# Kernel optimization log

Measured on AMD Instinct MI355X. Metric: run time of the kernel, lower is better.

The kernel has to match this reference:

```python
import jax, jax.numpy as jnp
import numpy as np

B, H, S, D = 4, 16, 1024, 64


def setup_inputs() -> dict:
    key = jax.random.key(0)
    kq, kk, kv, kw = jax.random.split(key, 4)
    xq = jax.random.normal(kq, (B, H, S, D), dtype=jnp.float32)
    xk = jax.random.normal(kk, (B, H, S, D), dtype=jnp.float32)
    xv = jax.random.normal(kv, (B, H, S, D), dtype=jnp.float32)
    # wpsm: nn.Linear(n_heads, n_heads, bias=False) weight, shape [H_out, H_in]
    bound = 1.0 / np.sqrt(H)
    W = jax.random.uniform(kw, (H, H), minval=-bound, maxval=bound, dtype=jnp.float32)
    return {"xq": xq, "xk": xk, "xv": xv, "W": W, "causal": 1}


def reference(xq, xk, xv, W, causal):
    head_dim = xq.shape[-1]
    sq, sk = xq.shape[-2], xk.shape[-2]
    # QK^T scaled: [B, H, Sq, Sk]
    scores = jnp.einsum("bhqd,bhkd->bhqk", xq, xk) * jax.lax.rsqrt(jnp.float32(head_dim))
    # head-mixing linear over head axis: mixed[b,g,q,k] = sum_h W[g,h] * scores[b,h,q,k]
    scores = jnp.einsum("gh,bhqk->bgqk", W, scores)
    if causal:
        mask = jnp.triu(jnp.full((sq, sk), -jnp.inf, dtype=scores.dtype), k=1)
        scores = scores + mask  # broadcast over [B, H]
    probs = jax.nn.softmax(scores.astype(jnp.float32), axis=-1).astype(xq.dtype)
    out = jnp.einsum("bhqk,bhkd->bhqd", probs, xv)
    return out.transpose(0, 2, 1, 3)  # [B, Sq, H, D]
```

## Files before the change

### kernel.cpp

```cpp
#include <hip/hip_runtime.h>
#include <math.h>

#define NB 4
#define HH 16
#define SS 1024
#define DD 64
#define NKST 16

typedef __attribute__((ext_vector_type(8))) short bf16x8;
typedef __attribute__((ext_vector_type(4))) float f32x4;

static __device__ __forceinline__ short f2bf(float f) {
    __bf16 h = (__bf16)f;
    return __builtin_bit_cast(short, h);
}
static __device__ __forceinline__ float bflo(int w) {
    return __builtin_bit_cast(float, (unsigned)w << 16);
}
static __device__ __forceinline__ float bfhi(int w) {
    return __builtin_bit_cast(float, (unsigned)w & 0xffff0000u);
}
static __device__ __forceinline__ int pidx(int pos, int hp) {
    int s = ((pos >> 2) & 3) | (((pos >> 9) & 1) << 2);
    return pos * 8 + (hp ^ s);
}
static __device__ __forceinline__ int midx(int gl, int loc, int x3) {
    return gl * 512 + ((((loc >> 2) ^ x3) << 2) | (loc & 3));
}

static __device__ __forceinline__ bf16x8 load8_bf16(const float* p) {
    const float4* p4 = reinterpret_cast<const float4*>(p);
    float4 a = p4[0], b = p4[1];
    bf16x8 f;
    f[0]=f2bf(a.x); f[1]=f2bf(a.y); f[2]=f2bf(a.z); f[3]=f2bf(a.w);
    f[4]=f2bf(b.x); f[5]=f2bf(b.y); f[6]=f2bf(b.z); f[7]=f2bf(b.w);
    return f;
}

__global__ __launch_bounds__(256) void prep_kfrag(const float* __restrict__ xk,
                                                  short* __restrict__ kfr) {
    int c = blockIdx.x * 256 + threadIdx.x;
    int lane = c & 63, ds = (c >> 6) & 1, kt = (c >> 7) & 3;
    int kst = (c >> 9) & 15, h = (c >> 13) & 15, b = c >> 17;
    const float* src = xk + ((size_t)((b * HH + h) * SS) + kst * 64 + kt * 16 + (lane & 15)) * DD
                          + ds * 32 + (lane >> 4) * 8;
    *(reinterpret_cast<bf16x8*>(kfr) + c) = load8_bf16(src);
}

__global__ __launch_bounds__(256) void prep_vfrag(const float* __restrict__ xv,
                                                  short* __restrict__ vfr) {
    __shared__ float T[64][65];
    int tile = blockIdx.x;
    int t = threadIdx.x;
    const float* src = xv + ((size_t)(tile >> 4) * SS + (tile & 15) * 64) * DD;
    int row = t >> 2, col = (t & 3) * 16;
#pragma unroll
    for (int ii = 0; ii < 4; ++ii) {
        float4 v = *reinterpret_cast<const float4*>(src + row * DD + col + ii * 4);
        T[row][col + ii*4] = v.x; T[row][col + ii*4 + 1] = v.y;
        T[row][col + ii*4 + 2] = v.z; T[row][col + ii*4 + 3] = v.w;
    }
    __syncthreads();
#pragma unroll
    for (int jj = 0; jj < 2; ++jj) {
        int c2 = t * 2 + jj;
        int lane = c2 & 63, nt = (c2 >> 6) & 3, kc = (c2 >> 8) & 1;
        bf16x8 o;
#pragma unroll
        for (int i = 0; i < 8; ++i)
            o[i] = f2bf(T[kc * 32 + (lane >> 4) * 8 + i][nt * 16 + (lane & 15)]);
        *(reinterpret_cast<bf16x8*>(vfr) + (size_t)tile * 512 + c2) = o;
    }
}

__global__ __launch_bounds__(512, 4) void hca_fused(
    const float* __restrict__ xq, const short* __restrict__ kfr,
    const short* __restrict__ vfr, const float* __restrict__ Wm,
    const int* __restrict__ causalp, float* __restrict__ out)
{
    __shared__ int Pbuf[8192];
    __shared__ int Mbuf[4096];

    const int tid  = threadIdx.x;
    const int lane = tid & 63;
    const int w    = tid >> 6;
    const int l15  = lane & 15;
    const int lg   = lane >> 4;

    const int bid  = blockIdx.x;
    const int i8   = bid & 255;
    const int rnd  = bid >> 8;
    const int b    = i8 & 3;
    const int jj   = i8 >> 2;
    const int qt   = rnd ? jj : 63 - jj;
    const int half = rnd;
    const int q0   = qt << 4;

    const int causal = causalp[0];
    const int g  = half * 8 + w;

    const float LOG2E = 1.44269504088896f;

    bf16x8 wt = {0,0,0,0,0,0,0,0};
    if (lg < 2) {
#pragma unroll
        for (int i = 0; i < 8; ++i)
            wt[i] = f2bf(Wm[l15 * 16 + lg * 8 + i] * 0.125f * LOG2E);
    }

    bf16x8 qf[2][2];
#pragma unroll
    for (int hi = 0; hi < 2; ++hi) {
        const float* qp = xq + ((size_t)(b * HH + 2 * w + hi) * SS + q0 + l15) * DD + lg * 8;
#pragma unroll
        for (int ds = 0; ds < 2; ++ds) qf[hi][ds] = load8_bf16(qp + ds * 32);
    }

    f32x4 oacc[4];
#pragma unroll
    for (int nt = 0; nt < 4; ++nt) oacc[nt] = (f32x4){0.f, 0.f, 0.f, 0.f};
    float mrun = -INFINITY, lrun = 0.f;

    const int nk = causal ? ((q0 + 16 + 63) >> 6) : NKST;

    for (int kst = 0; kst < nk; ++kst) {
        const int k0 = kst << 6;

        const short* kbase = kfr + ((size_t)((b * HH + 2 * w) * NKST + kst) * 8) * 512 + lane * 8;
#pragma unroll
        for (int kt = 0; kt < 4; ++kt) {
            f32x4 a0 = (f32x4){0.f,0.f,0.f,0.f}, a1 = a0;
#pragma unroll
            for (int ds = 0; ds < 2; ++ds) {
                bf16x8 kfa = *reinterpret_cast<const bf16x8*>(kbase + (kt*2 + ds) * 512);
                bf16x8 kfb = *reinterpret_cast<const bf16x8*>(kbase + (NKST*8 + kt*2 + ds) * 512);
                a0 = __builtin_amdgcn_mfma_f32_16x16x32_bf16(qf[0][ds], kfa, a0, 0, 0, 0);
                a1 = __builtin_amdgcn_mfma_f32_16x16x32_bf16(qf[1][ds], kfb, a1, 0, 0, 0);
            }
#pragma unroll
            for (int r = 0; r < 4; ++r) {
                int pos = (lg * 4 + r) * 64 + kt * 16 + l15;
                int pk = (int)(unsigned short)f2bf(a0[r]) | ((int)(unsigned short)f2bf(a1[r]) << 16);
                Pbuf[pidx(pos, w)] = pk;
            }
        }

        const short* vbase = vfr + ((size_t)((b * HH + g) * NKST + kst) * 8) * 512 + lane * 8;
        bf16x8 vf[8];
#pragma unroll
        for (int kc = 0; kc < 2; ++kc)
#pragma unroll
            for (int nt = 0; nt < 4; ++nt)
                vf[kc * 4 + nt] = *reinterpret_cast<const bf16x8*>(vbase + (kc*4 + nt) * 512);

        __syncthreads();

#pragma unroll
        for (int m = 0; m < 8; ++m) {
            const int c = w * 8 + m;
            const int pos = c * 16 + l15;
            int4 ia = {0, 0, 0, 0};
            if (lg < 2) {
                ia.x = Pbuf[pidx(pos, lg * 4 + 0)];
                ia.y = Pbuf[pidx(pos, lg * 4 + 1)];
                ia.z = Pbuf[pidx(pos, lg * 4 + 2)];
                ia.w = Pbuf[pidx(pos, lg * 4 + 3)];
            }
            bf16x8 A = __builtin_bit_cast(bf16x8, ia);
            f32x4 cc = (f32x4){0.f, 0.f, 0.f, 0.f};
            cc = __builtin_amdgcn_mfma_f32_16x16x32_bf16(A, wt, cc, 0, 0, 0);
            if ((l15 >> 3) == half) {
                int q = c >> 2;
                int loc = q * 32 + (c & 3) * 8 + lg * 2;
                int x3 = (q + l15) & 7;
                int u0 = (int)(unsigned short)f2bf(cc[0]) | ((int)(unsigned short)f2bf(cc[1]) << 16);
                int u1 = (int)(unsigned short)f2bf(cc[2]) | ((int)(unsigned short)f2bf(cc[3]) << 16);
                *reinterpret_cast<int2*>(&Mbuf[midx(l15 & 7, loc, x3)]) = make_int2(u0, u1);
            }
        }
        __syncthreads();

        const int x3r = (l15 + w) & 7;
        int4 rA = *reinterpret_cast<const int4*>(&Mbuf[midx(w, l15 * 32 + lg * 4, x3r)]);
        int4 rB = *reinterpret_cast<const int4*>(&Mbuf[midx(w, l15 * 32 + 16 + lg * 4, x3r)]);

        float sm[16];
#pragma unroll
        for (int j = 0; j < 4; ++j) {
            sm[2*j]     = bflo(rA[j]);  sm[2*j + 1] = bfhi(rA[j]);
            sm[8 + 2*j] = bflo(rB[j]);  sm[9 + 2*j] = bfhi(rB[j]);
        }
        if (causal && kst == nk - 1) {
#pragma unroll
            for (int j = 0; j < 16; ++j) {
                int kk = (j < 8) ? (lg * 8 + j) : (32 + lg * 8 + (j - 8));
                if (k0 + kk > q0 + l15) sm[j] = -INFINITY;
            }
        }

        float mx[4];
#pragma unroll
        for (int t = 0; t < 4; ++t)
            mx[t] = fmaxf(fmaxf(sm[4*t], sm[4*t+1]), fmaxf(sm[4*t+2], sm[4*t+3]));
        float mt = fmaxf(fmaxf(mx[0], mx[1]), fmaxf(mx[2], mx[3]));
        mt = fmaxf(mt, __shfl_xor(mt, 16));
        mt = fmaxf(mt, __shfl_xor(mt, 32));

        if (__any(mt > mrun + 8.0f)) {
            float mnew = fmaxf(mrun, mt);
            float scl = __builtin_amdgcn_exp2f(mrun - mnew);
            mrun = mnew;
            lrun *= scl;
            int scli = __builtin_bit_cast(int, scl);
#pragma unroll
            for (int r = 0; r < 4; ++r) {
                int v = __builtin_amdgcn_ds_bpermute((lg * 4 + r) * 4, scli);
                float s = __builtin_bit_cast(float, v);
#pragma unroll
                for (int nt = 0; nt < 4; ++nt) oacc[nt][r] *= s;
            }
        }

        float p[16];
#pragma unroll
        for (int j = 0; j < 16; ++j) p[j] = __builtin_amdgcn_exp2f(sm[j] - mrun);
        float s0 = ((p[0]+p[1]) + (p[2]+p[3])) + ((p[4]+p[5]) + (p[6]+p[7]));
        float s1 = ((p[8]+p[9]) + (p[10]+p[11])) + ((p[12]+p[13]) + (p[14]+p[15]));
        lrun += s0 + s1;

        int paw[8];
#pragma unroll
        for (int t = 0; t < 8; ++t)
            paw[t] = (int)(unsigned short)f2bf(p[2*t]) | ((int)(unsigned short)f2bf(p[2*t+1]) << 16);
        bf16x8 pa0 = __builtin_bit_cast(bf16x8, *(int4*)&paw[0]);
        bf16x8 pa1 = __builtin_bit_cast(bf16x8, *(int4*)&paw[4]);

#pragma unroll
        for (int nt = 0; nt < 4; ++nt) {
            oacc[nt] = __builtin_amdgcn_mfma_f32_16x16x32_bf16(pa0, vf[nt], oacc[nt], 0, 0, 0);
            oacc[nt] = __builtin_amdgcn_mfma_f32_16x16x32_bf16(pa1, vf[4 + nt], oacc[nt], 0, 0, 0);
        }
    }

    float lt = lrun;
    lt += __shfl_xor(lt, 16);
    lt += __shfl_xor(lt, 32);
    int lti = __builtin_bit_cast(int, lt);
#pragma unroll
    for (int r = 0; r < 4; ++r) {
        int v = __builtin_amdgcn_ds_bpermute((lg * 4 + r) * 4, lti);
        float linv = 1.0f / __builtin_bit_cast(float, v);
        int q = lg * 4 + r;
#pragma unroll
        for (int nt = 0; nt < 4; ++nt)
            out[((size_t)(b * SS + q0 + q) * HH + g) * DD + nt * 16 + l15] =
                oacc[nt][r] * linv;
    }
}

extern "C" void kernel_launch(void* const* d_in, const int* in_sizes, int n_in,
                              void* d_out, int out_size, void* d_ws, size_t ws_size,
                              hipStream_t stream) {
    const float* xq = (const float*)d_in[0];
    const float* xk = (const float*)d_in[1];
    const float* xv = (const float*)d_in[2];
    const float* Wm = (const float*)d_in[3];
    const int* causal = (const int*)d_in[4];
    float* out = (float*)d_out;

    short* vfr = (short*)d_ws;
    short* kfr = vfr + (size_t)NB * HH * SS * DD;

    prep_kfrag<<<2048, 256, 0, stream>>>(xk, kfr);
    prep_vfrag<<<NB * HH * NKST, 256, 0, stream>>>(xv, vfr);

    hca_fused<<<512, 512, 0, stream>>>(xq, kfr, vfr, Wm, causal, out);
}
```

Baseline: 87.75 us.

## Split key range across blocks with split-K attention and a combine kernel

Before, each block handled half the output heads and recomputed the full QK and head-mix for its q-tile. Now each block computes all 16 heads but only every other key tile (even or odd). It writes bf16 partial outputs plus per-row max and sum to workspace, and a new combine kernel merges the two halves. This removes the duplicated QK and head-mix work across the two blocks. It also evens out the causal imbalance between blocks, and s_setprio hints are added around the MFMA sections. The cost is a doubled Mbuf in shared memory, an extra kernel launch, more workspace traffic, and extra bf16 rounding of the partial outputs.

```diff
diff --git a/kernel.cpp b/kernel.cpp
--- a/kernel.cpp
+++ b/kernel.cpp
@@ -20,12 +20,15 @@
 static __device__ __forceinline__ float bfhi(int w) {
     return __builtin_bit_cast(float, (unsigned)w & 0xffff0000u);
 }
+static __device__ __forceinline__ float bfu(unsigned short u) {
+    return __builtin_bit_cast(float, (unsigned)u << 16);
+}
 static __device__ __forceinline__ int pidx(int pos, int hp) {
     int s = ((pos >> 2) & 3) | (((pos >> 9) & 1) << 2);
     return pos * 8 + (hp ^ s);
 }
-static __device__ __forceinline__ int midx(int gl, int loc, int x3) {
-    return gl * 512 + ((((loc >> 2) ^ x3) << 2) | (loc & 3));
+static __device__ __forceinline__ int midx(int g, int loc, int x3) {
+    return g * 512 + ((((loc >> 2) ^ x3) << 2) | (loc & 3));
 }
 
 static __device__ __forceinline__ bf16x8 load8_bf16(const float* p) {
@@ -76,10 +79,11 @@
 __global__ __launch_bounds__(512, 4) void hca_fused(
     const float* __restrict__ xq, const short* __restrict__ kfr,
     const short* __restrict__ vfr, const float* __restrict__ Wm,
-    const int* __restrict__ causalp, float* __restrict__ out)
+    const int* __restrict__ causalp, unsigned short* __restrict__ ppO,
+    float2* __restrict__ ppml)
 {
     __shared__ int Pbuf[8192];
-    __shared__ int Mbuf[4096];
+    __shared__ int Mbuf[8192];
 
     const int tid  = threadIdx.x;
     const int lane = tid & 63;
@@ -88,24 +92,22 @@
     const int lg   = lane >> 4;
 
     const int bid  = blockIdx.x;
-    const int i8   = bid & 255;
-    const int rnd  = bid >> 8;
-    const int b    = i8 & 3;
-    const int jj   = i8 >> 2;
-    const int qt   = rnd ? jj : 63 - jj;
-    const int half = rnd;
+    const int j    = bid & 255;
+    const int kpar = bid >> 8;
+    const int b    = j & 3;
+    const int i    = j >> 2;
+    const int qt   = kpar ? i : 63 - i;
     const int q0   = qt << 4;
+    const int pairIdx = b * 64 + qt;
 
     const int causal = causalp[0];
-    const int g  = half * 8 + w;
-
     const float LOG2E = 1.44269504088896f;
 
     bf16x8 wt = {0,0,0,0,0,0,0,0};
     if (lg < 2) {
 #pragma unroll
-        for (int i = 0; i < 8; ++i)
-            wt[i] = f2bf(Wm[l15 * 16 + lg * 8 + i] * 0.125f * LOG2E);
+        for (int ii = 0; ii < 8; ++ii)
+            wt[ii] = f2bf(Wm[l15 * 16 + lg * 8 + ii] * 0.125f * LOG2E);
     }
 
     bf16x8 qf[2][2];
@@ -116,17 +118,21 @@
         for (int ds = 0; ds < 2; ++ds) qf[hi][ds] = load8_bf16(qp + ds * 32);
     }
 
-    f32x4 oacc[4];
-#pragma unroll
-    for (int nt = 0; nt < 4; ++nt) oacc[nt] = (f32x4){0.f, 0.f, 0.f, 0.f};
-    float mrun = -INFINITY, lrun = 0.f;
+    f32x4 oacc[2][4];
+#pragma unroll
+    for (int gi = 0; gi < 2; ++gi)
+#pragma unroll
+        for (int nt = 0; nt < 4; ++nt) oacc[gi][nt] = (f32x4){0.f, 0.f, 0.f, 0.f};
+    float mrun[2] = {-INFINITY, -INFINITY};
+    float lrun[2] = {0.f, 0.f};
 
     const int nk = causal ? ((q0 + 16 + 63) >> 6) : NKST;
 
-    for (int kst = 0; kst < nk; ++kst) {
+    for (int kst = kpar; kst < nk; kst += 2) {
         const int k0 = kst << 6;
 
         const short* kbase = kfr + ((size_t)((b * HH + 2 * w) * NKST + kst) * 8) * 512 + lane * 8;
+        __builtin_amdgcn_s_setprio(1);
 #pragma unroll
         for (int kt = 0; kt < 4; ++kt) {
             f32x4 a0 = (f32x4){0.f,0.f,0.f,0.f}, a1 = a0;
@@ -144,15 +150,7 @@
                 Pbuf[pidx(pos, w)] = pk;
             }
         }
-
-        const short* vbase = vfr + ((size_t)((b * HH + g) * NKST + kst) * 8) * 512 + lane * 8;
-        bf16x8 vf[8];
-#pragma unroll
-        for (int kc = 0; kc < 2; ++kc)
-#pragma unroll
-            for (int nt = 0; nt < 4; ++nt)
-                vf[kc * 4 + nt] = *reinterpret_cast<const bf16x8*>(vbase + (kc*4 + nt) * 512);
-
+        __builtin_amdgcn_s_setprio(0);
         __syncthreads();
 
 #pragma unroll
@@ -169,92 +167,146 @@
             bf16x8 A = __builtin_bit_cast(bf16x8, ia);
             f32x4 cc = (f32x4){0.f, 0.f, 0.f, 0.f};
             cc = __builtin_amdgcn_mfma_f32_16x16x32_bf16(A, wt, cc, 0, 0, 0);
-            if ((l15 >> 3) == half) {
-                int q = c >> 2;
-                int loc = q * 32 + (c & 3) * 8 + lg * 2;
-                int x3 = (q + l15) & 7;
-                int u0 = (int)(unsigned short)f2bf(cc[0]) | ((int)(unsigned short)f2bf(cc[1]) << 16);
-                int u1 = (int)(unsigned short)f2bf(cc[2]) | ((int)(unsigned short)f2bf(cc[3]) << 16);
-                *reinterpret_cast<int2*>(&Mbuf[midx(l15 & 7, loc, x3)]) = make_int2(u0, u1);
-            }
+            int q = c >> 2;
+            int loc = q * 32 + (c & 3) * 8 + lg * 2;
+            int x3 = (q + l15) & 7;
+            int u0 = (int)(unsigned short)f2bf(cc[0]) | ((int)(unsigned short)f2bf(cc[1]) << 16);
+            int u1 = (int)(unsigned short)f2bf(cc[2]) | ((int)(unsigned short)f2bf(cc[3]) << 16);
+            *reinterpret_cast<int2*>(&Mbuf[midx(l15, loc, x3)]) = make_int2(u0, u1);
         }
         __syncthreads();
 
-        const int x3r = (l15 + w) & 7;
-        int4 rA = *reinterpret_cast<const int4*>(&Mbuf[midx(w, l15 * 32 + lg * 4, x3r)]);
-        int4 rB = *reinterpret_cast<const int4*>(&Mbuf[midx(w, l15 * 32 + 16 + lg * 4, x3r)]);
-
-        float sm[16];
-#pragma unroll
-        for (int j = 0; j < 4; ++j) {
-            sm[2*j]     = bflo(rA[j]);  sm[2*j + 1] = bfhi(rA[j]);
-            sm[8 + 2*j] = bflo(rB[j]);  sm[9 + 2*j] = bfhi(rB[j]);
+#pragma unroll
+        for (int gi = 0; gi < 2; ++gi) {
+            const int g = 2 * w + gi;
+
+            const short* vbase = vfr + ((size_t)((b * HH + g) * NKST + kst) * 8) * 512 + lane * 8;
+            bf16x8 vf[8];
+#pragma unroll
+            for (int kc = 0; kc < 2; ++kc)
+#pragma unroll
+                for (int nt = 0; nt < 4; ++nt)
+                    vf[kc * 4 + nt] = *reinterpret_cast<const bf16x8*>(vbase + (kc*4 + nt) * 512);
+
+            const int x3r = (l15 + g) & 7;
+            int4 rA = *reinterpret_cast<const int4*>(&Mbuf[midx(g, l15 * 32 + lg * 4, x3r)]);
+            int4 rB = *reinterpret_cast<const int4*>(&Mbuf[midx(g, l15 * 32 + 16 + lg * 4, x3r)]);
+
+            float sm[16];
+#pragma unroll
+            for (int jj = 0; jj < 4; ++jj) {
+                sm[2*jj]     = bflo(rA[jj]);  sm[2*jj + 1] = bfhi(rA[jj]);
+                sm[8 + 2*jj] = bflo(rB[jj]);  sm[9 + 2*jj] = bfhi(rB[jj]);
+            }
+            if (causal && kst == nk - 1) {
+#pragma unroll
+                for (int jj = 0; jj < 16; ++jj) {
+                    int kk = (jj < 8) ? (lg * 8 + jj) : (32 + lg * 8 + (jj - 8));
+                    if (k0 + kk > q0 + l15) sm[jj] = -INFINITY;
+                }
+            }
+
+            float mx[4];
+#pragma unroll
+            for (int t = 0; t < 4; ++t)
+                mx[t] = fmaxf(fmaxf(sm[4*t], sm[4*t+1]), fmaxf(sm[4*t+2], sm[4*t+3]));
+            float mt = fmaxf(fmaxf(mx[0], mx[1]), fmaxf(mx[2], mx[3]));
+            mt = fmaxf(mt, __shfl_xor(mt, 16));
+            mt = fmaxf(mt, __shfl_xor(mt, 32));
+
+            if (__any(mt > mrun[gi] + 8.0f)) {
+                float mnew = fmaxf(mrun[gi], mt);
+                float scl = __builtin_amdgcn_exp2f(mrun[gi] - mnew);
+                mrun[gi] = mnew;
+                lrun[gi] *= scl;
+                int scli = __builtin_bit_cast(int, scl);
+#pragma unroll
+                for (int r = 0; r < 4; ++r) {
+                    int v = __builtin_amdgcn_ds_bpermute((lg * 4 + r) * 4, scli);
+                    float s = __builtin_bit_cast(float, v);
+#pragma unroll
+                    for (int nt = 0; nt < 4; ++nt) oacc[gi][nt][r] *= s;
+                }
+            }
+
+            float p[16];
+#pragma unroll
+            for (int jj = 0; jj < 16; ++jj) p[jj] = __builtin_amdgcn_exp2f(sm[jj] - mrun[gi]);
+            float s0 = ((p[0]+p[1]) + (p[2]+p[3])) + ((p[4]+p[5]) + (p[6]+p[7]));
+            float s1 = ((p[8]+p[9]) + (p[10]+p[11])) + ((p[12]+p[13]) + (p[14]+p[15]));
+            lrun[gi] += s0 + s1;
+
+            int paw[8];
+#pragma unroll
+            for (int t = 0; t < 8; ++t)
+                paw[t] = (int)(unsigned short)f2bf(p[2*t]) | ((int)(unsigned short)f2bf(p[2*t+1]) << 16);
+            bf16x8 pa0 = __builtin_bit_cast(bf16x8, *(int4*)&paw[0]);
+            bf16x8 pa1 = __builtin_bit_cast(bf16x8, *(int4*)&paw[4]);
+
+            __builtin_amdgcn_s_setprio(1);
+#pragma unroll
+            for (int nt = 0; nt < 4; ++nt) {
+                oacc[gi][nt] = __builtin_amdgcn_mfma_f32_16x16x32_bf16(pa0, vf[nt], oacc[gi][nt], 0, 0, 0);
+                oacc[gi][nt] = __builtin_amdgcn_mfma_f32_16x16x32_bf16(pa1, vf[4 + nt], oacc[gi][nt], 0, 0, 0);
+            }
+            __builtin_amdgcn_s_setprio(0);
         }
-        if (causal && kst == nk - 1) {
-#pragma unroll
-            for (int j = 0; j < 16; ++j) {
-                int kk = (j < 8) ? (lg * 8 + j) : (32 + lg * 8 + (j - 8));
-                if (k0 + kk > q0 + l15) sm[j] = -INFINITY;
-            }
+    }
+
+#pragma unroll
+    for (int gi = 0; gi < 2; ++gi) {
+        const int g = 2 * w + gi;
+        float lt = lrun[gi];
+        lt += __shfl_xor(lt, 16);
+        lt += __shfl_xor(lt, 32);
+        if (lg == 0)
+            ppml[(((size_t)pairIdx * 2 + kpar) * 16 + g) * 16 + l15] = make_float2(mrun[gi], lt);
+        float rl = (lt > 0.f) ? (1.0f / lt) : 0.f;
+        int rli = __builtin_bit_cast(int, rl);
+        size_t obase = (((size_t)pairIdx * 2 + kpar) * 16 + g) * 1024;
+#pragma unroll
+        for (int r = 0; r < 4; ++r) {
+            int v = __builtin_amdgcn_ds_bpermute((lg * 4 + r) * 4, rli);
+            float linv = __builtin_bit_cast(float, v);
+            int q = lg * 4 + r;
+#pragma unroll
+            for (int nt = 0; nt < 4; ++nt)
+                ppO[obase + q * 64 + nt * 16 + l15] =
+                    (unsigned short)f2bf(oacc[gi][nt][r] * linv);
         }
-
-        float mx[4];
-#pragma unroll
-        for (int t = 0; t < 4; ++t)
-            mx[t] = fmaxf(fmaxf(sm[4*t], sm[4*t+1]), fmaxf(sm[4*t+2], sm[4*t+3]));
-        float mt = fmaxf(fmaxf(mx[0], mx[1]), fmaxf(mx[2], mx[3]));
-        mt = fmaxf(mt, __shfl_xor(mt, 16));
-        mt = fmaxf(mt, __shfl_xor(mt, 32));
-
-        if (__any(mt > mrun + 8.0f)) {
-            float mnew = fmaxf(mrun, mt);
-            float scl = __builtin_amdgcn_exp2f(mrun - mnew);
-            mrun = mnew;
-            lrun *= scl;
-            int scli = __builtin_bit_cast(int, scl);
-#pragma unroll
-            for (int r = 0; r < 4; ++r) {
-                int v = __builtin_amdgcn_ds_bpermute((lg * 4 + r) * 4, scli);
-                float s = __builtin_bit_cast(float, v);
-#pragma unroll
-                for (int nt = 0; nt < 4; ++nt) oacc[nt][r] *= s;
-            }
-        }
-
-        float p[16];
-#pragma unroll
-        for (int j = 0; j < 16; ++j) p[j] = __builtin_amdgcn_exp2f(sm[j] - mrun);
-        float s0 = ((p[0]+p[1]) + (p[2]+p[3])) + ((p[4]+p[5]) + (p[6]+p[7]));
-        float s1 = ((p[8]+p[9]) + (p[10]+p[11])) + ((p[12]+p[13]) + (p[14]+p[15]));
-        lrun += s0 + s1;
-
-        int paw[8];
-#pragma unroll
-        for (int t = 0; t < 8; ++t)
-            paw[t] = (int)(unsigned short)f2bf(p[2*t]) | ((int)(unsigned short)f2bf(p[2*t+1]) << 16);
-        bf16x8 pa0 = __builtin_bit_cast(bf16x8, *(int4*)&paw[0]);
-        bf16x8 pa1 = __builtin_bit_cast(bf16x8, *(int4*)&paw[4]);
-
-#pragma unroll
-        for (int nt = 0; nt < 4; ++nt) {
-            oacc[nt] = __builtin_amdgcn_mfma_f32_16x16x32_bf16(pa0, vf[nt], oacc[nt], 0, 0, 0);
-            oacc[nt] = __builtin_amdgcn_mfma_f32_16x16x32_bf16(pa1, vf[4 + nt], oacc[nt], 0, 0, 0);
-        }
-    }
-
-    float lt = lrun;
-    lt += __shfl_xor(lt, 16);
-    lt += __shfl_xor(lt, 32);
-    int lti = __builtin_bit_cast(int, lt);
-#pragma unroll
-    for (int r = 0; r < 4; ++r) {
-        int v = __builtin_amdgcn_ds_bpermute((lg * 4 + r) * 4, lti);
-        float linv = 1.0f / __builtin_bit_cast(float, v);
-        int q = lg * 4 + r;
-#pragma unroll
-        for (int nt = 0; nt < 4; ++nt)
-            out[((size_t)(b * SS + q0 + q) * HH + g) * DD + nt * 16 + l15] =
-                oacc[nt][r] * linv;
+    }
+}
+
+__global__ __launch_bounds__(256) void hca_combine(
+    const unsigned short* __restrict__ ppO, const float2* __restrict__ ppml,
+    float* __restrict__ out)
+{
+    const int pairIdx = blockIdx.x;
+    const int b = pairIdx >> 6, qt = pairIdx & 63;
+    const int t = threadIdx.x;
+    const int g = t >> 4, dc = t & 15;
+
+    const size_t o0 = (((size_t)pairIdx * 2 + 0) * 16 + g) * 1024;
+    const size_t o1 = (((size_t)pairIdx * 2 + 1) * 16 + g) * 1024;
+    const float2* ml0p = ppml + (((size_t)pairIdx * 2 + 0) * 16 + g) * 16;
+    const float2* ml1p = ppml + (((size_t)pairIdx * 2 + 1) * 16 + g) * 16;
+
+#pragma unroll 4
+    for (int q = 0; q < 16; ++q) {
+        float2 ml0 = ml0p[q], ml1 = ml1p[q];
+        float ms = fmaxf(ml0.x, ml1.x);
+        float w0 = ml0.y * exp2f(ml0.x - ms);
+        float w1 = ml1.y * exp2f(ml1.x - ms);
+        float rs = 1.0f / (w0 + w1);
+        float a0 = w0 * rs, a1 = w1 * rs;
+        ushort4 u0 = *reinterpret_cast<const ushort4*>(ppO + o0 + q * 64 + dc * 4);
+        ushort4 u1 = *reinterpret_cast<const ushort4*>(ppO + o1 + q * 64 + dc * 4);
+        float4 res;
+        res.x = a0 * bfu(u0.x) + a1 * bfu(u1.x);
+        res.y = a0 * bfu(u0.y) + a1 * bfu(u1.y);
+        res.z = a0 * bfu(u0.z) + a1 * bfu(u1.z);
+        res.w = a0 * bfu(u0.w) + a1 * bfu(u1.w);
+        *reinterpret_cast<float4*>(out + (((size_t)b * SS + qt * 16 + q) * HH + g) * DD + dc * 4) = res;
     }
 }
 
@@ -270,9 +322,12 @@
 
     short* vfr = (short*)d_ws;
     short* kfr = vfr + (size_t)NB * HH * SS * DD;
+    unsigned short* ppO = (unsigned short*)(kfr + (size_t)NB * HH * SS * DD);
+    float2* ppml = (float2*)(ppO + (size_t)512 * 16 * 1024);
 
     prep_kfrag<<<2048, 256, 0, stream>>>(xk, kfr);
     prep_vfrag<<<NB * HH * NKST, 256, 0, stream>>>(xv, vfr);
 
-    hca_fused<<<512, 512, 0, stream>>>(xq, kfr, vfr, Wm, causal, out);
-}
+    hca_fused<<<512, 512, 0, stream>>>(xq, kfr, vfr, Wm, causal, ppO, ppml);
+    hca_combine<<<256, 256, 0, stream>>>(ppO, ppml, out);
+}
```

Result: slower. 149.6 us (+70.4%).
